# Optimization experiments

Hardware: AMD Instinct MI355X
Metric: run time of the kernel (lower is better)

The kernel has to match this reference:

```python
import jax, jax.numpy as jnp
import numpy as np

H = 128            # hidden_dim
R = 16             # num_rbf
L = 3              # num_atom_encoder_layers
LAT = 32           # latent_dim
NUM_ATOM_TYPES = 64
CUTOFF = 5.0       # atom_cutoff
N_RES = 2048
DEG = 16           # avg radius-graph degree
_PATTERN = np.array([19, 20, 21, 22, 23, 24, 25, 22])  # ragged atoms/residue, mean 22


def setup_inputs() -> dict:
    key = jax.random.key(0)
    ks = jax.random.split(key, 16)
    apr = np.tile(_PATTERN, N_RES // len(_PATTERN))        # (N,) atoms per residue
    A = int(apr.sum())                                     # 45056 atoms
    E = A * DEG                                            # 720896 edges
    rng = np.random.default_rng(0)

    def gl(k, shape, fan_in):
        return jax.random.normal(k, shape, jnp.float32) * (fan_in ** -0.5)

    return {
        "atom_coords": jax.random.normal(ks[0], (A, 3), jnp.float32) * 10.0,
        "atom_types": jax.random.randint(ks[1], (A,), 0, NUM_ATOM_TYPES),
        "residue_indices": jnp.asarray(np.repeat(np.arange(N_RES), apr)),
        "residue_types": jax.random.randint(ks[2], (N_RES,), 0, 4),
        "atoms_per_residue": jnp.asarray(apr),
        "edge_src": jnp.asarray(rng.integers(0, A, E)),
        "edge_dst": jnp.asarray(rng.integers(0, A, E)),
        # learned parameters
        "atom_embed": gl(ks[3], (NUM_ATOM_TYPES, H), 1.0),
        "residue_embed": gl(ks[4], (4, H), 1.0),
        "We1": gl(ks[5], (L, 2 * H + R, H), 2 * H + R), "be1": jnp.zeros((L, H)),
        "We2": gl(ks[6], (L, H, H), H), "be2": jnp.zeros((L, H)),
        "Wh1": gl(ks[7], (L, 2 * H, H), 2 * H), "bh1": jnp.zeros((L, H)),
        "Wh2": gl(ks[8], (L, H, H), H), "bh2": jnp.zeros((L, H)),
        "Wq": gl(ks[9], (H, H), H), "bq": jnp.zeros((H,)),
        "Wk": gl(ks[10], (H, H), H), "bk": jnp.zeros((H,)),
        "Wv": gl(ks[11], (H, H), H), "bv": jnp.zeros((H,)),
        "Wmu": gl(ks[12], (H, LAT), H), "bmu": jnp.zeros((LAT,)),
        "Wlv": gl(ks[13], (H, LAT), H) * 0.01, "blv": jnp.full((LAT,), -2.0),
    }


def reference(atom_coords, atom_types, residue_indices, residue_types,
              atoms_per_residue, edge_src, edge_dst,
              atom_embed, residue_embed,
              We1, be1, We2, be2, Wh1, bh1, Wh2, bh2,
              Wq, bq, Wk, bk, Wv, bv, Wmu, bmu, Wlv, blv):
    A = atom_coords.shape[0]
    N = residue_types.shape[0]
    coords = atom_coords - atom_coords.mean(0, keepdims=True)  # center_coords

    # Gaussian radial basis expansion of edge distances
    d = jnp.linalg.norm(coords[edge_src] - coords[edge_dst], axis=-1)  # (E,)
    centers = jnp.linspace(0.0, CUTOFF, R)
    gamma = (R / CUTOFF) ** 2
    edge_attr = jnp.exp(-gamma * (d[:, None] - centers) ** 2)          # (E,R)

    # atom features: atom-type embed + residue-type embed scattered to atoms
    res_emb = residue_embed[residue_types]                             # (N,H)
    h = atom_embed[atom_types] + res_emb[residue_indices]              # (A,H)

    # EGNN layers (update_coords=False): message MLP -> sum-agg -> residual node MLP
    for l in range(L):
        m = jnp.concatenate([h[edge_src], h[edge_dst], edge_attr], axis=-1)  # (E,2H+R)
        m = jax.nn.silu(m @ We1[l] + be1[l])
        m = jax.nn.silu(m @ We2[l] + be2[l])                                  # (E,H)
        agg = jax.ops.segment_sum(m, edge_dst, num_segments=A)               # (A,H)
        u = jnp.concatenate([h, agg], axis=-1)                               # (A,2H)
        u = jax.nn.silu(u @ Wh1[l] + bh1[l])
        h = h + (u @ Wh2[l] + bh2[l])

    # segment (per-residue) attention pooling of atoms -> residues
    q = res_emb @ Wq + bq                                              # (N,H)
    k = h @ Wk + bk                                                    # (A,H)
    v = h @ Wv + bv                                                    # (A,H)
    scores = jnp.sum(q[residue_indices] * k, axis=-1) * (H ** -0.5)    # (A,)
    smax = jax.ops.segment_max(scores, residue_indices, num_segments=N)
    ex = jnp.exp(scores - smax[residue_indices])
    denom = jax.ops.segment_sum(ex, residue_indices, num_segments=N)
    w = ex / denom[residue_indices]
    pooled = jax.ops.segment_sum(w[:, None] * v, residue_indices, num_segments=N)  # (N,H)

    mu = pooled @ Wmu + bmu
    logvar = jnp.clip(pooled @ Wlv + blv, -10.0, 2.0)
    return mu, logvar
```

## Files before the change

kernel.cpp:

```cpp
#include <hip/hip_runtime.h>
#include <hip/hip_bf16.h>

#define H 128
#define LATD 32

typedef __attribute__((ext_vector_type(8))) _Float16 half8t;
typedef __attribute__((ext_vector_type(4))) _Float16 half4t;
typedef __attribute__((ext_vector_type(2))) _Float16 half2t;
typedef __attribute__((ext_vector_type(8))) unsigned short u16x8;
typedef __attribute__((ext_vector_type(4))) float f32x4;

#define OFF_RBF 0
#define OFF_W2  12288
#define OFF_PROJ 61440
#define OFF_H1  159744
#define OFF_H2  258048
#define OFF_KV  307200
#define OFF_RBF16 339968
#define WP_TOTAL 346112

__device__ __forceinline__ float silu_f(float x) {
  return x * __builtin_amdgcn_rcpf(1.0f + __expf(-x));
}
__device__ __forceinline__ unsigned short f16u(float x) {
  _Float16 hh = (_Float16)x;
  return *(unsigned short*)&hh;
}

__global__ void k_init_h(const float* __restrict__ atom_embed,
                         const float* __restrict__ residue_embed,
                         const int* __restrict__ atype,
                         const int* __restrict__ ridx,
                         const int* __restrict__ rtype,
                         float* __restrict__ h, unsigned short* __restrict__ hb,
                         int* __restrict__ starts, int A) {
  int i = blockIdx.x * blockDim.x + threadIdx.x;
  if (i >= A * H) return;
  int a = i >> 7, j = i & 127;
  int r = ridx[a];
  float v = atom_embed[atype[a] * H + j] + residue_embed[rtype[r] * H + j];
  h[i] = v;
  hb[i] = f16u(v);
  if (j == 0 && (a == 0 || ridx[a - 1] != r)) starts[r] = a;
}

__global__ void k_dist(const float* __restrict__ coords,
                       const int* __restrict__ esrc, const int* __restrict__ edst,
                       float* __restrict__ dbuf, int* __restrict__ cnt, int E) {
  int e = blockIdx.x * blockDim.x + threadIdx.x;
  if (e >= E) return;
  int s = esrc[e], t = edst[e];
  float dx = coords[3*s+0] - coords[3*t+0];
  float dy = coords[3*s+1] - coords[3*t+1];
  float dz = coords[3*s+2] - coords[3*t+2];
  dbuf[e] = sqrtf(dx*dx + dy*dy + dz*dz);
  atomicAdd(&cnt[t], 1);
}

__global__ __launch_bounds__(1024) void k_scanA(const int* __restrict__ cnt,
                                                int* __restrict__ cursor,
                                                int* __restrict__ bsum, int A) {
  __shared__ int buf[1024];
  int tid = threadIdx.x;
  int i = blockIdx.x * 1024 + tid;
  int v = (i < A) ? cnt[i] : 0;
  buf[tid] = v;
  __syncthreads();
  #pragma unroll
  for (int off = 1; off < 1024; off <<= 1) {
    int nv = (tid >= off) ? buf[tid - off] : 0;
    __syncthreads();
    buf[tid] += nv;
    __syncthreads();
  }
  if (i < A) cursor[i] = buf[tid] - v;
  if (tid == 1023) bsum[blockIdx.x] = buf[1023];
}

__global__ void k_scanB(int* __restrict__ bsum, int nb) {
  int lane = threadIdx.x;
  int v = (lane < nb) ? bsum[lane] : 0;
  int s = v;
  #pragma unroll
  for (int off = 1; off < 64; off <<= 1) {
    int nv = __shfl_up(s, off);
    if (lane >= off) s += nv;
  }
  if (lane < nb) bsum[lane] = s - v;
}

__global__ void k_scanC(int* __restrict__ cursor, const int* __restrict__ bsum, int A) {
  int i = blockIdx.x * blockDim.x + threadIdx.x;
  if (i < A) cursor[i] += bsum[i >> 10];
}

__global__ void k_scatter(const int* __restrict__ edst, int* __restrict__ cursor,
                          int* __restrict__ eperm, int E) {
  int e = blockIdx.x * blockDim.x + threadIdx.x;
  if (e >= E) return;
  int p = atomicAdd(&cursor[edst[e]], 1);
  eperm[p] = e;
}

__global__ void k_pack(const float* __restrict__ We1, const float* __restrict__ We2,
                       const float* __restrict__ Wh1, const float* __restrict__ Wh2,
                       const float* __restrict__ Wk,  const float* __restrict__ Wv,
                       unsigned short* __restrict__ wp) {
  int t = blockIdx.x * blockDim.x + threadIdx.x;
  if (t >= WP_TOTAL) return;
  if (t < OFF_W2) {
    wp[t] = 0;
  } else if (t < OFF_PROJ) {
    int u = t - OFF_W2; int layer = u / 16384, idx = u % 16384;
    int i = idx & 7, lane = (idx >> 3) & 63, ct = (idx >> 9) & 7, kt = idx >> 12;
    int k = kt * 32 + (lane >> 4) * 8 + i, c = ct * 16 + (lane & 15);
    const float* src = We2 + (size_t)layer * 128 * H;
    wp[t] = f16u(src[(size_t)k * H + c]);
  } else if (t < OFF_H1) {
    int u = t - OFF_PROJ; int layer = u / 32768, idx = u % 32768;
    int i = idx & 7, lane = (idx >> 3) & 63, ct = (idx >> 9) & 15, kt = idx >> 13;
    int k = kt * 32 + (lane >> 4) * 8 + i, c = ct * 16 + (lane & 15);
    const float* src = We1 + (size_t)layer * 272 * H;
    float v = (c < 128) ? src[(size_t)k * H + c] : src[(size_t)(128 + k) * H + (c - 128)];
    wp[t] = f16u(v);
  } else if (t < OFF_H2) {
    int u = t - OFF_H1; int layer = u / 32768, idx = u % 32768;
    int i = idx & 7, lane = (idx >> 3) & 63, ct = (idx >> 9) & 7, kt = idx >> 12;
    int k = kt * 32 + (lane >> 4) * 8 + i, c = ct * 16 + (lane & 15);
    const float* src = Wh1 + (size_t)layer * 256 * H;
    wp[t] = f16u(src[(size_t)k * H + c]);
  } else if (t < OFF_KV) {
    int u = t - OFF_H2; int layer = u / 16384, idx = u % 16384;
    int i = idx & 7, lane = (idx >> 3) & 63, ct = (idx >> 9) & 7, kt = idx >> 12;
    int k = kt * 32 + (lane >> 4) * 8 + i, c = ct * 16 + (lane & 15);
    const float* src = Wh2 + (size_t)layer * 128 * H;
    wp[t] = f16u(src[(size_t)k * H + c]);
  } else if (t < OFF_RBF16) {
    int idx = t - OFF_KV;
    int i = idx & 7, lane = (idx >> 3) & 63, ct = (idx >> 9) & 15, kt = idx >> 13;
    int k = kt * 32 + (lane >> 4) * 8 + i, c = ct * 16 + (lane & 15);
    float v = (c < 128) ? Wk[(size_t)k * H + c] : Wv[(size_t)k * H + (c - 128)];
    wp[t] = f16u(v);
  } else {
    int u = t - OFF_RBF16; int layer = u / 2048, idx = u % 2048;
    int i = idx & 3, lane = (idx >> 2) & 63, ct = idx >> 8;
    int k = (lane >> 4) * 4 + i;
    int c = ct * 16 + (lane & 15);
    const float* src = We1 + (size_t)layer * 272 * H;
    wp[t] = f16u(src[(size_t)(256 + k) * H + c]);
  }
}

__global__ __launch_bounds__(256) void k_proj(
    const unsigned short* __restrict__ hb, const unsigned short* __restrict__ Wp,
    unsigned short* __restrict__ Ph, int A, const float* __restrict__ bias,
    float* __restrict__ agg_zero) {
  const int tid = threadIdx.x, l = tid & 63, wv = tid >> 6;
  const int lr = l & 15, lk = (l >> 4) * 8;
  const int a0 = blockIdx.x * 64;
  if (agg_zero) {
    int a = a0 + (tid >> 2);
    if (a < A) {
      float4 z = {0.f, 0.f, 0.f, 0.f};
      float4* dst = (float4*)(agg_zero + (size_t)a * H) + (tid & 3) * 8;
      #pragma unroll
      for (int i = 0; i < 8; ++i) dst[i] = z;
    }
  }
  f32x4 acc[4][4] = {};
  #pragma unroll
  for (int kt = 0; kt < 4; ++kt) {
    half8t a[4], b[4];
    #pragma unroll
    for (int rt = 0; rt < 4; ++rt) {
      int row = a0 + rt * 16 + lr; if (row >= A) row = A - 1;
      a[rt] = *(const half8t*)&hb[(size_t)row * H + kt * 32 + lk];
    }
    #pragma unroll
    for (int ci = 0; ci < 4; ++ci)
      b[ci] = *(const half8t*)&Wp[(((size_t)kt * 16 + wv * 4 + ci) * 64 + l) * 8];
    #pragma unroll
    for (int rt = 0; rt < 4; ++rt)
      #pragma unroll
      for (int ci = 0; ci < 4; ++ci)
        acc[rt][ci] = __builtin_amdgcn_mfma_f32_16x16x32_f16(a[rt], b[ci], acc[rt][ci], 0, 0, 0);
  }
  #pragma unroll
  for (int rt = 0; rt < 4; ++rt)
    #pragma unroll
    for (int ci = 0; ci < 4; ++ci) {
      int col = (wv * 4 + ci) * 16 + lr;
      float bb = bias ? bias[col] : 0.0f;
      #pragma unroll
      for (int rr = 0; rr < 4; ++rr) {
        int row = a0 + rt * 16 + (l >> 4) * 4 + rr;
        if (row < A) Ph[(size_t)row * 256 + col] = f16u(acc[rt][ci][rr] + bb);
      }
    }
}

#define ES 136

__global__ __launch_bounds__(256) void k_edge_mfma(
    const unsigned short* __restrict__ Ph, const float* __restrict__ dbuf,
    const int* __restrict__ esrc, const int* __restrict__ edst,
    const int* __restrict__ eperm,
    const unsigned short* __restrict__ Wr16, const float* __restrict__ be1,
    const unsigned short* __restrict__ W2p, const float* __restrict__ be2,
    float* __restrict__ agg, int E) {
  __shared__ __align__(16) unsigned short SH[64 * ES];
  __shared__ int dstv[64];
  __shared__ float dval[64];

  const int tid = threadIdx.x;
  const int e0 = blockIdx.x * 64;
  const int l = tid & 63, wv = tid >> 6;
  const int lr = l & 15, lk = (l >> 4) * 8, g4 = (l >> 4) * 4;
  const int ct0 = wv * 2;

  {
    const int r = tid >> 2, qt = tid & 3;
    int e = e0 + r;
    int ec = (e < E) ? e : (E - 1);
    int es = eperm[ec];
    int s = esrc[es], t = edst[es];
    if (qt == 0) {
      dstv[r] = (e < E) ? t : -1;
      dval[r] = dbuf[es];
    }
    const half8t* ps = (const half8t*)(Ph + (size_t)s * 256);
    const half8t* pt = (const half8t*)(Ph + (size_t)t * 256 + 128);
    half8t* pr = (half8t*)&SH[r * ES];
    #pragma unroll
    for (int i = 0; i < 4; ++i)
      pr[qt * 4 + i] = ps[qt * 4 + i] + pt[qt * 4 + i];
  }
  __syncthreads();

  f32x4 acc[2][4];
  #pragma unroll
  for (int cj = 0; cj < 2; ++cj) {
    int cbase = (ct0 + cj) * 16 + g4;
    #pragma unroll
    for (int et = 0; et < 4; ++et) {
      half4t p4 = *(const half4t*)&SH[(et * 16 + lr) * ES + cbase];
      acc[cj][et][0] = (float)p4[0];
      acc[cj][et][1] = (float)p4[1];
      acc[cj][et][2] = (float)p4[2];
      acc[cj][et][3] = (float)p4[3];
    }
  }
  {
    half4t br[4];
    #pragma unroll
    for (int et = 0; et < 4; ++et) {
      float d = dval[et * 16 + lr];
      #pragma unroll
      for (int i = 0; i < 4; ++i) {
        float dd = d - (float)(g4 + i) * (5.0f / 15.0f);
        br[et][i] = (_Float16)__expf(-10.24f * dd * dd);
      }
    }
    half4t ar[2];
    #pragma unroll
    for (int cj = 0; cj < 2; ++cj)
      ar[cj] = *(const half4t*)&Wr16[(((size_t)(ct0 + cj)) * 64 + l) * 4];
    #pragma unroll
    for (int et = 0; et < 4; ++et)
      #pragma unroll
      for (int cj = 0; cj < 2; ++cj)
        acc[cj][et] = __builtin_amdgcn_mfma_f32_16x16x16f16(ar[cj], br[et], acc[cj][et], 0, 0, 0);
  }
  __syncthreads();

  #pragma unroll
  for (int cj = 0; cj < 2; ++cj) {
    f32x4 b1v = *(const f32x4*)&be1[(ct0 + cj) * 16 + g4];
    #pragma unroll
    for (int et = 0; et < 4; ++et) {
      half4t m4;
      #pragma unroll
      for (int rr = 0; rr < 4; ++rr)
        m4[rr] = (_Float16)silu_f(acc[cj][et][rr] + b1v[rr]);
      *(half4t*)&SH[(et * 16 + lr) * ES + (ct0 + cj) * 16 + g4] = m4;
    }
  }
  __syncthreads();

  f32x4 acc2[2][4] = {};
  #pragma unroll
  for (int kt = 0; kt < 4; ++kt) {
    half8t a2[2], b2[4];
    #pragma unroll
    for (int cj = 0; cj < 2; ++cj)
      a2[cj] = *(const half8t*)&W2p[(((size_t)kt * 8 + ct0 + cj) * 64 + l) * 8];
    #pragma unroll
    for (int et = 0; et < 4; ++et)
      b2[et] = *(const half8t*)&SH[(et * 16 + lr) * ES + kt * 32 + lk];
    #pragma unroll
    for (int cj = 0; cj < 2; ++cj)
      #pragma unroll
      for (int et = 0; et < 4; ++et)
        acc2[cj][et] = __builtin_amdgcn_mfma_f32_16x16x32_f16(a2[cj], b2[et], acc2[cj][et], 0, 0, 0);
  }
  __syncthreads();

  #pragma unroll
  for (int cj = 0; cj < 2; ++cj) {
    f32x4 b2v = *(const f32x4*)&be2[(ct0 + cj) * 16 + g4];
    #pragma unroll
    for (int et = 0; et < 4; ++et) {
      half4t m4;
      #pragma unroll
      for (int rr = 0; rr < 4; ++rr)
        m4[rr] = (_Float16)silu_f(acc2[cj][et][rr] + b2v[rr]);
      *(half4t*)&SH[(et * 16 + lr) * ES + (ct0 + cj) * 16 + g4] = m4;
    }
  }
  __syncthreads();

  {
    int cp = tid & 63, qr = tid >> 6;
    int rbeg = qr * 16, rend = rbeg + 16;
    float a0 = 0.f, a1 = 0.f;
    int prev = -1;
    for (int r = rbeg; r < rend; ++r) {
      int dv = dstv[r];
      half2t v = *(const half2t*)&SH[r * ES + cp * 2];
      if (dv != prev) {
        if (prev >= 0) {
          atomicAdd(&agg[(size_t)prev * H + cp * 2], a0);
          atomicAdd(&agg[(size_t)prev * H + cp * 2 + 1], a1);
        }
        a0 = a1 = 0.f;
        prev = dv;
      }
      if (dv >= 0) { a0 += (float)v[0]; a1 += (float)v[1]; }
    }
    if (prev >= 0) {
      atomicAdd(&agg[(size_t)prev * H + cp * 2], a0);
      atomicAdd(&agg[(size_t)prev * H + cp * 2 + 1], a1);
    }
  }
}

#define NXS 264
#define M1S 136

__global__ __launch_bounds__(256) void k_node_mfma(
    float* __restrict__ h, unsigned short* __restrict__ hb,
    const float* __restrict__ agg,
    const unsigned short* __restrict__ W1p, const float* __restrict__ bh1,
    const unsigned short* __restrict__ W2p, const float* __restrict__ bh2, int A) {
  __shared__ __align__(16) unsigned short Xs[32 * NXS];
  __shared__ __align__(16) unsigned short Us[32 * M1S];
  const int tid = threadIdx.x;
  const int a0 = blockIdx.x * 32;
  {
    const int r = tid >> 3, oct = tid & 7;
    int a = a0 + r; if (a >= A) a = A - 1;
    const u16x8* hr = (const u16x8*)(hb + (size_t)a * H);
    u16x8* xr = (u16x8*)&Xs[r * NXS];
    xr[oct * 2]     = hr[oct * 2];
    xr[oct * 2 + 1] = hr[oct * 2 + 1];
    const float4* ar = (const float4*)(agg + (size_t)a * H);
    u16x8 tmp[2];
    unsigned short* tp = (unsigned short*)tmp;
    #pragma unroll
    for (int i = 0; i < 4; ++i) {
      float4 av = ar[oct * 4 + i];
      tp[i*4+0] = f16u(av.x); tp[i*4+1] = f16u(av.y);
      tp[i*4+2] = f16u(av.z); tp[i*4+3] = f16u(av.w);
    }
    xr[16 + oct * 2]     = tmp[0];
    xr[16 + oct * 2 + 1] = tmp[1];
  }
  __syncthreads();

  const int l = tid & 63, wv = tid >> 6;
  const int lr = l & 15, lk = (l >> 4) * 8;
  const int ct0 = wv * 2;
  const int c0 = ct0 * 16 + lr, c1 = c0 + 16;
  const float b1a = bh1[c0], b1b = bh1[c1];
  const float b2a = bh2[c0], b2b = bh2[c1];

  f32x4 acc[2][2] = {};
  #pragma unroll
  for (int kt = 0; kt < 8; ++kt) {
    half8t a[2], b[2];
    #pragma unroll
    for (int rt = 0; rt < 2; ++rt)
      a[rt] = *(const half8t*)&Xs[(rt * 16 + lr) * NXS + kt * 32 + lk];
    #pragma unroll
    for (int j = 0; j < 2; ++j)
      b[j] = *(const half8t*)&W1p[(((size_t)kt * 8 + ct0 + j) * 64 + l) * 8];
    #pragma unroll
    for (int rt = 0; rt < 2; ++rt)
      #pragma unroll
      for (int j = 0; j < 2; ++j)
        acc[rt][j] = __builtin_amdgcn_mfma_f32_16x16x32_f16(a[rt], b[j], acc[rt][j], 0, 0, 0);
  }
  #pragma unroll
  for (int rt = 0; rt < 2; ++rt)
    #pragma unroll
    for (int j = 0; j < 2; ++j) {
      float bb = j ? b1b : b1a;
      int col = (ct0 + j) * 16 + lr;
      #pragma unroll
      for (int rr = 0; rr < 4; ++rr) {
        int row = rt * 16 + (l >> 4) * 4 + rr;
        Us[row * M1S + col] = f16u(silu_f(acc[rt][j][rr] + bb));
      }
    }
  __syncthreads();

  f32x4 acc2[2][2] = {};
  #pragma unroll
  for (int kt = 0; kt < 4; ++kt) {
    half8t a[2], b[2];
    #pragma unroll
    for (int rt = 0; rt < 2; ++rt)
      a[rt] = *(const half8t*)&Us[(rt * 16 + lr) * M1S + kt * 32 + lk];
    #pragma unroll
    for (int j = 0; j < 2; ++j)
      b[j] = *(const half8t*)&W2p[(((size_t)kt * 8 + ct0 + j) * 64 + l) * 8];
    #pragma unroll
    for (int rt = 0; rt < 2; ++rt)
      #pragma unroll
      for (int j = 0; j < 2; ++j)
        acc2[rt][j] = __builtin_amdgcn_mfma_f32_16x16x32_f16(a[rt], b[j], acc2[rt][j], 0, 0, 0);
  }
  #pragma unroll
  for (int rt = 0; rt < 2; ++rt)
    #pragma unroll
    for (int j = 0; j < 2; ++j) {
      float bb = j ? b2b : b2a;
      int col = (ct0 + j) * 16 + lr;
      #pragma unroll
      for (int rr = 0; rr < 4; ++rr) {
        int row = rt * 16 + (l >> 4) * 4 + rr;
        int a = a0 + row;
        if (a < A) {
          size_t off = (size_t)a * H + col;
          float nh = h[off] + acc2[rt][j][rr] + bb;
          h[off] = nh;
          hb[off] = f16u(nh);
        }
      }
    }
}

__global__ void k_q4b(const float* __restrict__ residue_embed,
                      const float* __restrict__ Wq, const float* __restrict__ bq,
                      const float* __restrict__ bk, const float* __restrict__ bv,
                      float* __restrict__ q4, float* __restrict__ bkv) {
  int i = blockIdx.x * blockDim.x + threadIdx.x;
  if (i < 512) {
    int r = i >> 7, j = i & 127;
    const float* emb = residue_embed + (size_t)r * H;
    float s = bq[j];
    #pragma unroll 4
    for (int k = 0; k < H; ++k) s += emb[k] * Wq[(size_t)k*H + j];
    q4[i] = s;
  } else if (i < 768) {
    int t = i - 512;
    bkv[t] = (t < 128) ? bk[t] : bv[t - 128];
  }
}

__global__ void k_score(const unsigned short* __restrict__ kv,
                        const float* __restrict__ q4,
                        const int* __restrict__ ridx,
                        const int* __restrict__ rtype,
                        float* __restrict__ scores, int A) {
  int t = blockIdx.x * blockDim.x + threadIdx.x;
  int a = t >> 2, qt = t & 3;
  if (a >= A) return;
  const half8t* kr = (const half8t*)(kv + (size_t)a * 256 + qt * 32);
  const float* qrow = q4 + (size_t)rtype[ridx[a]] * H + qt * 32;
  float s = 0.f;
  #pragma unroll
  for (int i = 0; i < 4; ++i) {
    half8t kvv = kr[i];
    #pragma unroll
    for (int j = 0; j < 8; ++j) s += (float)kvv[j] * qrow[i * 8 + j];
  }
  s += __shfl_xor(s, 1);
  s += __shfl_xor(s, 2);
  if (qt == 0) scores[a] = s * 0.08838834764831845f;
}

__global__ __launch_bounds__(256) void k_pool(
    const float* __restrict__ scores,
    const unsigned short* __restrict__ kv, const int* __restrict__ starts,
    const int* __restrict__ apr, float* __restrict__ pooled, int N) {
  int r = blockIdx.x * 4 + (threadIdx.x >> 6);
  if (r >= N) return;
  int lane = threadIdx.x & 63;
  int s0 = starts[r], cnt = apr[r];
  float val = (lane < cnt) ? scores[s0 + lane] : -1e30f;
  float mx = val;
  #pragma unroll
  for (int off = 32; off; off >>= 1) mx = fmaxf(mx, __shfl_xor(mx, off));
  float ex = (lane < cnt) ? __expf(val - mx) : 0.0f;
  float sum = ex;
  #pragma unroll
  for (int off = 32; off; off >>= 1) sum += __shfl_xor(sum, off);
  float w = ex * __builtin_amdgcn_rcpf(sum);
  float p0 = 0.f, p1 = 0.f;
  for (int i = 0; i < cnt; ++i) {
    float wi = __shfl(w, i);
    const unsigned short* vr = kv + (size_t)(s0 + i) * 256 + 128;
    p0 += wi * (float)(*(const _Float16*)&vr[lane]);
    p1 += wi * (float)(*(const _Float16*)&vr[64 + lane]);
  }
  pooled[(size_t)r*H + lane] = p0;
  pooled[(size_t)r*H + 64 + lane] = p1;
}

__global__ void k_head(const float* __restrict__ pooled,
                       const float* __restrict__ Wmu, const float* __restrict__ bmu,
                       const float* __restrict__ Wlv, const float* __restrict__ blv,
                       float* __restrict__ out, int N) {
  int i = blockIdx.x * blockDim.x + threadIdx.x;
  if (i >= N * LATD) return;
  int r = i >> 5, j = i & 31;
  const float* p = pooled + (size_t)r * H;
  float smu = 0.f, slv = 0.f;
  #pragma unroll 4
  for (int k = 0; k < H; ++k) {
    float pv = p[k];
    smu += pv * Wmu[(size_t)k*LATD + j];
    slv += pv * Wlv[(size_t)k*LATD + j];
  }
  smu += bmu[j];
  slv += blv[j];
  slv = fminf(fmaxf(slv, -10.0f), 2.0f);
  out[i] = smu;
  out[(size_t)N*LATD + i] = slv;
}

extern "C" void kernel_launch(void* const* d_in, const int* in_sizes, int n_in,
                              void* d_out, int out_size, void* d_ws, size_t ws_size,
                              hipStream_t stream) {
  const float* coords        = (const float*)d_in[0];
  const int*   atype         = (const int*)d_in[1];
  const int*   ridx          = (const int*)d_in[2];
  const int*   rtype         = (const int*)d_in[3];
  const int*   apr           = (const int*)d_in[4];
  const int*   esrc          = (const int*)d_in[5];
  const int*   edst          = (const int*)d_in[6];
  const float* atom_embed    = (const float*)d_in[7];
  const float* residue_embed = (const float*)d_in[8];
  const float* We1 = (const float*)d_in[9];
  const float* be1 = (const float*)d_in[10];
  const float* We2 = (const float*)d_in[11];
  const float* be2 = (const float*)d_in[12];
  const float* Wh1 = (const float*)d_in[13];
  const float* bh1 = (const float*)d_in[14];
  const float* Wh2 = (const float*)d_in[15];
  const float* bh2 = (const float*)d_in[16];
  const float* Wq  = (const float*)d_in[17];
  const float* bq  = (const float*)d_in[18];
  const float* Wk  = (const float*)d_in[19];
  const float* bk  = (const float*)d_in[20];
  const float* Wv  = (const float*)d_in[21];
  const float* bv  = (const float*)d_in[22];
  const float* Wmu = (const float*)d_in[23];
  const float* bmu = (const float*)d_in[24];
  const float* Wlv = (const float*)d_in[25];
  const float* blv = (const float*)d_in[26];

  const int A = in_sizes[1];
  const int N = in_sizes[3];
  const int E = in_sizes[5];

  float* ws     = (float*)d_ws;
  float* h      = ws;
  float* agg    = h + (size_t)A * H;
  float* vbuf   = agg + (size_t)A * H;
  float* dbuf   = vbuf + (size_t)A * H;
  float* q4     = dbuf + (size_t)E;
  float* bkv    = q4 + 4 * H;
  float* pooled = bkv + 256;
  int*   starts = (int*)(pooled + (size_t)N * H);
  unsigned short* hbuf = (unsigned short*)(starts + N);
  int*   eperm  = (int*)(hbuf + (size_t)A * H);
  int*   cnt    = eperm + (size_t)E;
  int*   cursor = cnt + A;
  int*   bsum   = cursor + A;
  unsigned short* wp = (unsigned short*)(bsum + 64);
  unsigned short* Ph = (unsigned short*)vbuf;

  hipMemsetAsync(cnt, 0, (size_t)A * sizeof(int), stream);
  k_init_h<<<(A * H + 255) / 256, 256, 0, stream>>>(atom_embed, residue_embed,
                                                    atype, ridx, rtype, h, hbuf,
                                                    starts, A);
  k_dist<<<(E + 255) / 256, 256, 0, stream>>>(coords, esrc, edst, dbuf, cnt, E);
  k_pack<<<(WP_TOTAL + 255) / 256, 256, 0, stream>>>(We1, We2, Wh1, Wh2, Wk, Wv, wp);

  const int nb = (A + 1023) / 1024;
  k_scanA<<<nb, 1024, 0, stream>>>(cnt, cursor, bsum, A);
  k_scanB<<<1, 64, 0, stream>>>(bsum, nb);
  k_scanC<<<(A + 255) / 256, 256, 0, stream>>>(cursor, bsum, A);
  k_scatter<<<(E + 255) / 256, 256, 0, stream>>>(edst, cursor, eperm, E);

  const int egrid = (E + 63) / 64;
  for (int l = 0; l < 3; ++l) {
    k_proj<<<(A + 63) / 64, 256, 0, stream>>>(
        hbuf, wp + OFF_PROJ + (size_t)l * 32768, Ph, A, nullptr, agg);
    k_edge_mfma<<<egrid, 256, 0, stream>>>(
        Ph, dbuf, esrc, edst, eperm,
        wp + OFF_RBF16 + (size_t)l * 2048, be1 + (size_t)l * H,
        wp + OFF_W2    + (size_t)l * 16384, be2 + (size_t)l * H, agg, E);
    k_node_mfma<<<(A + 31) / 32, 256, 0, stream>>>(
        h, hbuf, agg,
        wp + OFF_H1 + (size_t)l * 32768, bh1 + (size_t)l * H,
        wp + OFF_H2 + (size_t)l * 16384, bh2 + (size_t)l * H, A);
  }

  k_q4b<<<3, 256, 0, stream>>>(residue_embed, Wq, bq, bk, bv, q4, bkv);
  unsigned short* kv = Ph;
  k_proj<<<(A + 63) / 64, 256, 0, stream>>>(hbuf, wp + OFF_KV, kv, A, bkv, nullptr);
  float* scores = dbuf;
  k_score<<<(A * 4 + 255) / 256, 256, 0, stream>>>(kv, q4, ridx, rtype, scores, A);
  k_pool<<<(N + 3) / 4, 256, 0, stream>>>(scores, kv, starts, apr, pooled, N);
  k_head<<<(N * LATD + 255) / 256, 256, 0, stream>>>(pooled, Wmu, bmu, Wlv, blv,
                                                     (float*)d_out, N);
}
```

Baseline: 618.1 us.

## Fuse node update with next-layer projection and init with first projection

Merges the node MLP kernel with the following layer's h projection (or the final K/V projection), reusing the updated h tile from shared memory instead of rereading it from global memory. The agg zeroing moves into the node kernel. Init embedding is fused with the first projection, and the scanC pass is folded into the scatter by adding the block offset there. Node tiles grow from 32 to 64 atoms, which raises shared memory and register use and may lower occupancy.

```diff
diff --git a/kernel.cpp b/kernel.cpp
--- a/kernel.cpp
+++ b/kernel.cpp
@@ -25,23 +25,6 @@
 __device__ __forceinline__ unsigned short f16u(float x) {
   _Float16 hh = (_Float16)x;
   return *(unsigned short*)&hh;
-}
-
-__global__ void k_init_h(const float* __restrict__ atom_embed,
-                         const float* __restrict__ residue_embed,
-                         const int* __restrict__ atype,
-                         const int* __restrict__ ridx,
-                         const int* __restrict__ rtype,
-                         float* __restrict__ h, unsigned short* __restrict__ hb,
-                         int* __restrict__ starts, int A) {
-  int i = blockIdx.x * blockDim.x + threadIdx.x;
-  if (i >= A * H) return;
-  int a = i >> 7, j = i & 127;
-  int r = ridx[a];
-  float v = atom_embed[atype[a] * H + j] + residue_embed[rtype[r] * H + j];
-  h[i] = v;
-  hb[i] = f16u(v);
-  if (j == 0 && (a == 0 || ridx[a - 1] != r)) starts[r] = a;
 }
 
 __global__ void k_dist(const float* __restrict__ coords,
@@ -89,16 +72,13 @@
   if (lane < nb) bsum[lane] = s - v;
 }
 
-__global__ void k_scanC(int* __restrict__ cursor, const int* __restrict__ bsum, int A) {
-  int i = blockIdx.x * blockDim.x + threadIdx.x;
-  if (i < A) cursor[i] += bsum[i >> 10];
-}
-
 __global__ void k_scatter(const int* __restrict__ edst, int* __restrict__ cursor,
+                          const int* __restrict__ bsum,
                           int* __restrict__ eperm, int E) {
   int e = blockIdx.x * blockDim.x + threadIdx.x;
   if (e >= E) return;
-  int p = atomicAdd(&cursor[edst[e]], 1);
+  int t = edst[e];
+  int p = atomicAdd(&cursor[t], 1) + bsum[t >> 10];
   eperm[p] = e;
 }
 
@@ -151,31 +131,57 @@
   }
 }
 
-__global__ __launch_bounds__(256) void k_proj(
-    const unsigned short* __restrict__ hb, const unsigned short* __restrict__ Wp,
-    unsigned short* __restrict__ Ph, int A, const float* __restrict__ bias,
-    float* __restrict__ agg_zero) {
-  const int tid = threadIdx.x, l = tid & 63, wv = tid >> 6;
+#define PS2 136
+
+__global__ __launch_bounds__(256) void k_init_proj(
+    const float* __restrict__ atom_embed, const float* __restrict__ residue_embed,
+    const int* __restrict__ atype, const int* __restrict__ ridx,
+    const int* __restrict__ rtype,
+    float* __restrict__ h, unsigned short* __restrict__ hb,
+    int* __restrict__ starts, float* __restrict__ agg,
+    const unsigned short* __restrict__ Wp, unsigned short* __restrict__ Ph, int A) {
+  __shared__ __align__(16) unsigned short Xp[64 * PS2];
+  const int tid = threadIdx.x;
+  const int a0 = blockIdx.x * 64;
+  {
+    const int r = tid >> 2, qt = tid & 3;
+    int a = a0 + r;
+    int ac = (a < A) ? a : (A - 1);
+    int ri = ridx[ac];
+    const float* ae = atom_embed + (size_t)atype[ac] * H + qt * 32;
+    const float* re = residue_embed + (size_t)rtype[ri] * H + qt * 32;
+    if (a < A) {
+      if (qt == 0 && (a == 0 || ridx[a - 1] != ri)) starts[ri] = a;
+      float4 z = {0.f, 0.f, 0.f, 0.f};
+      float4* az = (float4*)(agg + (size_t)a * H + qt * 32);
+      #pragma unroll
+      for (int i = 0; i < 8; ++i) az[i] = z;
+      #pragma unroll
+      for (int j = 0; j < 32; ++j) {
+        float v = ae[j] + re[j];
+        h[(size_t)a * H + qt * 32 + j] = v;
+        unsigned short u = f16u(v);
+        hb[(size_t)a * H + qt * 32 + j] = u;
+        Xp[r * PS2 + qt * 32 + j] = u;
+      }
+    } else {
+      #pragma unroll
+      for (int j = 0; j < 32; ++j) {
+        float v = ae[j] + re[j];
+        Xp[r * PS2 + qt * 32 + j] = f16u(v);
+      }
+    }
+  }
+  __syncthreads();
+  const int l = tid & 63, wv = tid >> 6;
   const int lr = l & 15, lk = (l >> 4) * 8;
-  const int a0 = blockIdx.x * 64;
-  if (agg_zero) {
-    int a = a0 + (tid >> 2);
-    if (a < A) {
-      float4 z = {0.f, 0.f, 0.f, 0.f};
-      float4* dst = (float4*)(agg_zero + (size_t)a * H) + (tid & 3) * 8;
-      #pragma unroll
-      for (int i = 0; i < 8; ++i) dst[i] = z;
-    }
-  }
   f32x4 acc[4][4] = {};
   #pragma unroll
   for (int kt = 0; kt < 4; ++kt) {
     half8t a[4], b[4];
     #pragma unroll
-    for (int rt = 0; rt < 4; ++rt) {
-      int row = a0 + rt * 16 + lr; if (row >= A) row = A - 1;
-      a[rt] = *(const half8t*)&hb[(size_t)row * H + kt * 32 + lk];
-    }
+    for (int rt = 0; rt < 4; ++rt)
+      a[rt] = *(const half8t*)&Xp[(rt * 16 + lr) * PS2 + kt * 32 + lk];
     #pragma unroll
     for (int ci = 0; ci < 4; ++ci)
       b[ci] = *(const half8t*)&Wp[(((size_t)kt * 16 + wv * 4 + ci) * 64 + l) * 8];
@@ -190,11 +196,10 @@
     #pragma unroll
     for (int ci = 0; ci < 4; ++ci) {
       int col = (wv * 4 + ci) * 16 + lr;
-      float bb = bias ? bias[col] : 0.0f;
       #pragma unroll
       for (int rr = 0; rr < 4; ++rr) {
         int row = a0 + rt * 16 + (l >> 4) * 4 + rr;
-        if (row < A) Ph[(size_t)row * 256 + col] = f16u(acc[rt][ci][rr] + bb);
+        if (row < A) Ph[(size_t)row * 256 + col] = f16u(acc[rt][ci][rr]);
       }
     }
 }
@@ -344,108 +349,145 @@
   }
 }
 
-#define NXS 264
-#define M1S 136
-
-__global__ __launch_bounds__(256) void k_node_mfma(
+#define NXS2 264
+#define US2 136
+
+__global__ __launch_bounds__(256) void k_node_proj(
     float* __restrict__ h, unsigned short* __restrict__ hb,
-    const float* __restrict__ agg,
+    float* __restrict__ agg, int zero_agg,
     const unsigned short* __restrict__ W1p, const float* __restrict__ bh1,
-    const unsigned short* __restrict__ W2p, const float* __restrict__ bh2, int A) {
-  __shared__ __align__(16) unsigned short Xs[32 * NXS];
-  __shared__ __align__(16) unsigned short Us[32 * M1S];
+    const unsigned short* __restrict__ W2p, const float* __restrict__ bh2,
+    const unsigned short* __restrict__ Wp, const float* __restrict__ pbias,
+    unsigned short* __restrict__ PhOut, int A) {
+  __shared__ __align__(16) unsigned short X2[64 * NXS2];
+  __shared__ __align__(16) unsigned short Us2[64 * US2];
   const int tid = threadIdx.x;
-  const int a0 = blockIdx.x * 32;
+  const int a0 = blockIdx.x * 64;
   {
-    const int r = tid >> 3, oct = tid & 7;
+    const int r = tid >> 2, qt = tid & 3;
     int a = a0 + r; if (a >= A) a = A - 1;
-    const u16x8* hr = (const u16x8*)(hb + (size_t)a * H);
-    u16x8* xr = (u16x8*)&Xs[r * NXS];
-    xr[oct * 2]     = hr[oct * 2];
-    xr[oct * 2 + 1] = hr[oct * 2 + 1];
-    const float4* ar = (const float4*)(agg + (size_t)a * H);
-    u16x8 tmp[2];
+    const u16x8* hr = (const u16x8*)(hb + (size_t)a * H + qt * 32);
+    u16x8* xr = (u16x8*)&X2[r * NXS2 + qt * 32];
+    xr[0] = hr[0]; xr[1] = hr[1]; xr[2] = hr[2]; xr[3] = hr[3];
+    float4* ar = (float4*)(agg + (size_t)a * H + qt * 32);
+    u16x8 tmp[4];
     unsigned short* tp = (unsigned short*)tmp;
     #pragma unroll
-    for (int i = 0; i < 4; ++i) {
-      float4 av = ar[oct * 4 + i];
+    for (int i = 0; i < 8; ++i) {
+      float4 av = ar[i];
       tp[i*4+0] = f16u(av.x); tp[i*4+1] = f16u(av.y);
       tp[i*4+2] = f16u(av.z); tp[i*4+3] = f16u(av.w);
     }
-    xr[16 + oct * 2]     = tmp[0];
-    xr[16 + oct * 2 + 1] = tmp[1];
+    u16x8* xg = (u16x8*)&X2[r * NXS2 + 128 + qt * 32];
+    xg[0] = tmp[0]; xg[1] = tmp[1]; xg[2] = tmp[2]; xg[3] = tmp[3];
+    if (zero_agg) {
+      float4 z = {0.f, 0.f, 0.f, 0.f};
+      #pragma unroll
+      for (int i = 0; i < 8; ++i) ar[i] = z;
+    }
   }
   __syncthreads();
 
   const int l = tid & 63, wv = tid >> 6;
   const int lr = l & 15, lk = (l >> 4) * 8;
   const int ct0 = wv * 2;
-  const int c0 = ct0 * 16 + lr, c1 = c0 + 16;
-  const float b1a = bh1[c0], b1b = bh1[c1];
-  const float b2a = bh2[c0], b2b = bh2[c1];
-
-  f32x4 acc[2][2] = {};
+
+  f32x4 acc[4][2] = {};
   #pragma unroll
   for (int kt = 0; kt < 8; ++kt) {
-    half8t a[2], b[2];
-    #pragma unroll
-    for (int rt = 0; rt < 2; ++rt)
-      a[rt] = *(const half8t*)&Xs[(rt * 16 + lr) * NXS + kt * 32 + lk];
+    half8t a[4], b[2];
+    #pragma unroll
+    for (int rt = 0; rt < 4; ++rt)
+      a[rt] = *(const half8t*)&X2[(rt * 16 + lr) * NXS2 + kt * 32 + lk];
     #pragma unroll
     for (int j = 0; j < 2; ++j)
       b[j] = *(const half8t*)&W1p[(((size_t)kt * 8 + ct0 + j) * 64 + l) * 8];
     #pragma unroll
-    for (int rt = 0; rt < 2; ++rt)
+    for (int rt = 0; rt < 4; ++rt)
       #pragma unroll
       for (int j = 0; j < 2; ++j)
         acc[rt][j] = __builtin_amdgcn_mfma_f32_16x16x32_f16(a[rt], b[j], acc[rt][j], 0, 0, 0);
   }
   #pragma unroll
-  for (int rt = 0; rt < 2; ++rt)
+  for (int rt = 0; rt < 4; ++rt)
     #pragma unroll
     for (int j = 0; j < 2; ++j) {
-      float bb = j ? b1b : b1a;
       int col = (ct0 + j) * 16 + lr;
+      float bb = bh1[col];
       #pragma unroll
       for (int rr = 0; rr < 4; ++rr) {
         int row = rt * 16 + (l >> 4) * 4 + rr;
-        Us[row * M1S + col] = f16u(silu_f(acc[rt][j][rr] + bb));
-      }
-    }
-  __syncthreads();
-
-  f32x4 acc2[2][2] = {};
+        Us2[row * US2 + col] = f16u(silu_f(acc[rt][j][rr] + bb));
+      }
+    }
+  __syncthreads();
+
+  f32x4 acc2[4][2] = {};
   #pragma unroll
   for (int kt = 0; kt < 4; ++kt) {
-    half8t a[2], b[2];
-    #pragma unroll
-    for (int rt = 0; rt < 2; ++rt)
-      a[rt] = *(const half8t*)&Us[(rt * 16 + lr) * M1S + kt * 32 + lk];
+    half8t a[4], b[2];
+    #pragma unroll
+    for (int rt = 0; rt < 4; ++rt)
+      a[rt] = *(const half8t*)&Us2[(rt * 16 + lr) * US2 + kt * 32 + lk];
     #pragma unroll
     for (int j = 0; j < 2; ++j)
       b[j] = *(const half8t*)&W2p[(((size_t)kt * 8 + ct0 + j) * 64 + l) * 8];
     #pragma unroll
-    for (int rt = 0; rt < 2; ++rt)
+    for (int rt = 0; rt < 4; ++rt)
       #pragma unroll
       for (int j = 0; j < 2; ++j)
         acc2[rt][j] = __builtin_amdgcn_mfma_f32_16x16x32_f16(a[rt], b[j], acc2[rt][j], 0, 0, 0);
   }
-  #pragma unroll
-  for (int rt = 0; rt < 2; ++rt)
+  unsigned short* NH = X2;
+  __syncthreads();
+  #pragma unroll
+  for (int rt = 0; rt < 4; ++rt)
     #pragma unroll
     for (int j = 0; j < 2; ++j) {
-      float bb = j ? b2b : b2a;
       int col = (ct0 + j) * 16 + lr;
+      float bb = bh2[col];
       #pragma unroll
       for (int rr = 0; rr < 4; ++rr) {
         int row = rt * 16 + (l >> 4) * 4 + rr;
         int a = a0 + row;
+        float nh = 0.0f;
         if (a < A) {
           size_t off = (size_t)a * H + col;
-          float nh = h[off] + acc2[rt][j][rr] + bb;
+          nh = h[off] + acc2[rt][j][rr] + bb;
           h[off] = nh;
           hb[off] = f16u(nh);
         }
+        NH[row * US2 + col] = f16u(nh);
+      }
+    }
+  __syncthreads();
+
+  f32x4 accp[4][4] = {};
+  #pragma unroll
+  for (int kt = 0; kt < 4; ++kt) {
+    half8t a[4], b[4];
+    #pragma unroll
+    for (int rt = 0; rt < 4; ++rt)
+      a[rt] = *(const half8t*)&NH[(rt * 16 + lr) * US2 + kt * 32 + lk];
+    #pragma unroll
+    for (int ci = 0; ci < 4; ++ci)
+      b[ci] = *(const half8t*)&Wp[(((size_t)kt * 16 + wv * 4 + ci) * 64 + l) * 8];
+    #pragma unroll
+    for (int rt = 0; rt < 4; ++rt)
+      #pragma unroll
+      for (int ci = 0; ci < 4; ++ci)
+        accp[rt][ci] = __builtin_amdgcn_mfma_f32_16x16x32_f16(a[rt], b[ci], accp[rt][ci], 0, 0, 0);
+  }
+  #pragma unroll
+  for (int rt = 0; rt < 4; ++rt)
+    #pragma unroll
+    for (int ci = 0; ci < 4; ++ci) {
+      int col = (wv * 4 + ci) * 16 + lr;
+      float bb = pbias ? pbias[col] : 0.0f;
+      #pragma unroll
+      for (int rr = 0; rr < 4; ++rr) {
+        int row = a0 + rt * 16 + (l >> 4) * 4 + rr;
+        if (row < A) PhOut[(size_t)row * 256 + col] = f16u(accp[rt][ci][rr] + bb);
       }
     }
 }
@@ -593,35 +635,34 @@
   unsigned short* Ph = (unsigned short*)vbuf;
 
   hipMemsetAsync(cnt, 0, (size_t)A * sizeof(int), stream);
-  k_init_h<<<(A * H + 255) / 256, 256, 0, stream>>>(atom_embed, residue_embed,
-                                                    atype, ridx, rtype, h, hbuf,
-                                                    starts, A);
+  k_pack<<<(WP_TOTAL + 255) / 256, 256, 0, stream>>>(We1, We2, Wh1, Wh2, Wk, Wv, wp);
+  k_q4b<<<3, 256, 0, stream>>>(residue_embed, Wq, bq, bk, bv, q4, bkv);
   k_dist<<<(E + 255) / 256, 256, 0, stream>>>(coords, esrc, edst, dbuf, cnt, E);
-  k_pack<<<(WP_TOTAL + 255) / 256, 256, 0, stream>>>(We1, We2, Wh1, Wh2, Wk, Wv, wp);
+  k_init_proj<<<(A + 63) / 64, 256, 0, stream>>>(
+      atom_embed, residue_embed, atype, ridx, rtype,
+      h, hbuf, starts, agg, wp + OFF_PROJ, Ph, A);
 
   const int nb = (A + 1023) / 1024;
   k_scanA<<<nb, 1024, 0, stream>>>(cnt, cursor, bsum, A);
   k_scanB<<<1, 64, 0, stream>>>(bsum, nb);
-  k_scanC<<<(A + 255) / 256, 256, 0, stream>>>(cursor, bsum, A);
-  k_scatter<<<(E + 255) / 256, 256, 0, stream>>>(edst, cursor, eperm, E);
+  k_scatter<<<(E + 255) / 256, 256, 0, stream>>>(edst, cursor, bsum, eperm, E);
 
   const int egrid = (E + 63) / 64;
+  unsigned short* kv = Ph;
   for (int l = 0; l < 3; ++l) {
-    k_proj<<<(A + 63) / 64, 256, 0, stream>>>(
-        hbuf, wp + OFF_PROJ + (size_t)l * 32768, Ph, A, nullptr, agg);
     k_edge_mfma<<<egrid, 256, 0, stream>>>(
         Ph, dbuf, esrc, edst, eperm,
         wp + OFF_RBF16 + (size_t)l * 2048, be1 + (size_t)l * H,
         wp + OFF_W2    + (size_t)l * 16384, be2 + (size_t)l * H, agg, E);
-    k_node_mfma<<<(A + 31) / 32, 256, 0, stream>>>(
-        h, hbuf, agg,
+    const unsigned short* Wnext =
+        (l < 2) ? (wp + OFF_PROJ + (size_t)(l + 1) * 32768) : (wp + OFF_KV);
+    k_node_proj<<<(A + 63) / 64, 256, 0, stream>>>(
+        h, hbuf, agg, (l < 2) ? 1 : 0,
         wp + OFF_H1 + (size_t)l * 32768, bh1 + (size_t)l * H,
-        wp + OFF_H2 + (size_t)l * 16384, bh2 + (size_t)l * H, A);
-  }
-
-  k_q4b<<<3, 256, 0, stream>>>(residue_embed, Wq, bq, bk, bv, q4, bkv);
-  unsigned short* kv = Ph;
-  k_proj<<<(A + 63) / 64, 256, 0, stream>>>(hbuf, wp + OFF_KV, kv, A, bkv, nullptr);
+        wp + OFF_H2 + (size_t)l * 16384, bh2 + (size_t)l * H,
+        Wnext, (l < 2) ? nullptr : bkv, Ph, A);
+  }
+
   float* scores = dbuf;
   k_score<<<(A * 4 + 255) / 256, 256, 0, stream>>>(kv, q4, ridx, rtype, scores, A);
   k_pool<<<(N + 3) / 4, 256, 0, stream>>>(scores, kv, starts, apr, pooled, N);
```

Result: faster. 590.3 us (-4.5%).
